# Kernel optimization log

Hardware: AMD Instinct MI355X
Metric: run time of the kernel (lower is better)

## Reference

```python
import jax, jax.numpy as jnp
import numpy as np
import math

COND_DIM = 64
HIDDEN = 128
NUM_SIN = 2
SQRT2 = 1.4142135623730951


def fused_leaky_relu(x, bias):
    # stylegan2 fused bias + leaky relu (slope 0.2) with sqrt(2) gain
    return jax.nn.leaky_relu(x + bias, negative_slope=0.2) * SQRT2


def equal_linear2(x, W, b, lr_mul=1.0, activation=False):
    scale = lr_mul / math.sqrt(W.shape[1])
    out = x @ (W * scale).T
    if activation:
        return fused_leaky_relu(out, b * lr_mul)
    return out + b * lr_mul


def coords_to_sinusoidals(x, num_sinusoidals=NUM_SIN, multiplier=2.0):
    # x: [P, 1] -> [P, 2*num_sinusoidals], freq_type='mult': freqs = multiplier**i
    freqs = multiplier ** jnp.arange(num_sinusoidals, dtype=x.dtype)  # [S]
    ang = x * freqs  # [P, S]
    return jnp.concatenate([jnp.sin(ang), jnp.cos(ang)], axis=-1)


def setup_inputs() -> dict:
    key = jax.random.key(0)
    ks = jax.random.split(key, 10)
    B, N = 64, 8192
    coord_in = 2 * NUM_SIN  # 4
    in1 = coord_in + COND_DIM  # 68
    in2 = HIDDEN + COND_DIM    # 192
    coords = jax.random.normal(ks[0], (B, N, 2), dtype=jnp.float32)
    c = jax.random.normal(ks[1], (B, N, COND_DIM), dtype=jnp.float32)
    # EqualLinear2 weights init uniform(-1,1)/lr_mul; last layer zero in torch,
    # use small random values here so gradients/outputs are non-trivial.
    Wx1 = jax.random.uniform(ks[2], (HIDDEN, in1), minval=-1.0, maxval=1.0)
    bx1 = jnp.zeros((HIDDEN,), jnp.float32)
    Wx2 = jax.random.uniform(ks[3], (2, in2), minval=-1.0, maxval=1.0) * 0.1
    bx2 = jnp.zeros((2,), jnp.float32)
    Wy1 = jax.random.uniform(ks[4], (HIDDEN, in1), minval=-1.0, maxval=1.0)
    by1 = jnp.zeros((HIDDEN,), jnp.float32)
    Wy2 = jax.random.uniform(ks[5], (2, in2), minval=-1.0, maxval=1.0) * 0.1
    by2 = jnp.zeros((2,), jnp.float32)
    return {"coords": coords, "c": c,
            "Wx1": Wx1, "bx1": bx1, "Wx2": Wx2, "bx2": bx2,
            "Wy1": Wy1, "by1": by1, "Wy2": Wy2, "by2": by2}


def reference(coords, c, Wx1, bx1, Wx2, bx2, Wy1, by1, Wy2, by2):
    initial_shape = coords.shape[:-1]
    coords2 = coords.reshape(-1, coords.shape[-1])  # [P, 2]
    cf = c.reshape(-1, c.shape[-1])                 # [P, cond]
    x = coords2[:, 0:1]
    y = coords2[:, 1:2]

    # x branch -> affine params for y
    h = coords_to_sinusoidals(x / 10.0)
    h = equal_linear2(jnp.concatenate([h, cf], -1), Wx1, bx1, activation=True)
    o = equal_linear2(jnp.concatenate([h, cf], -1), Wx2, bx2, activation=False)
    y_log_scale = jnp.clip(o[:, 0:1], -5.0, 5.0)
    y_bias = o[:, 1:2]
    y = y * jnp.exp(y_log_scale) + y_bias

    # y branch -> affine params for x
    h = coords_to_sinusoidals(y / 10.0)
    h = equal_linear2(jnp.concatenate([h, cf], -1), Wy1, by1, activation=True)
    o = equal_linear2(jnp.concatenate([h, cf], -1), Wy2, by2, activation=False)
    x_log_scale = jnp.clip(o[:, 0:1], -5.0, 5.0)
    x_bias = o[:, 1:2]
    x = x * jnp.exp(x_log_scale) + x_bias

    warped = jnp.concatenate([x, y], -1).reshape(*initial_shape, -1)
    log_jac = jnp.concatenate([x_log_scale + y_log_scale], -1)
    log_jac = (x_log_scale + y_log_scale).reshape(*initial_shape, -1)
    return warped, log_jac
```

## Files before the change

kernel.cpp:

```cpp
#include <hip/hip_runtime.h>

typedef unsigned short u16t;
typedef short short8 __attribute__((ext_vector_type(8)));
typedef float f32x4 __attribute__((ext_vector_type(4)));
typedef float f32x2 __attribute__((ext_vector_type(2)));

__device__ __forceinline__ u16t f2bf_rne(float f) {
  unsigned u = __builtin_bit_cast(unsigned, f);
  u += 0x7FFFu + ((u >> 16) & 1u);
  return (u16t)(u >> 16);
}
__device__ __forceinline__ unsigned pk2(float a, float b) {
  unsigned ua = __builtin_bit_cast(unsigned, a) + 0x8000u;
  unsigned ub = __builtin_bit_cast(unsigned, b) + 0x8000u;
  return (ua >> 16) | (ub & 0xFFFF0000u);
}
union S8U { short8 s; unsigned w[4]; };
__device__ __forceinline__ short8 pack8f(float4 a, float4 b) {
  S8U u;
  u.w[0] = pk2(a.x, a.y); u.w[1] = pk2(a.z, a.w);
  u.w[2] = pk2(b.x, b.y); u.w[3] = pk2(b.z, b.w);
  return u.s;
}

#define WS_WB  0
#define WS_BS  32768
#define WS_FQ  36864
#define LDS_BYTES 39936
#define WS_BC  39936
#define WS_BYTES 44032

__global__ void prep_kernel(const float* __restrict__ Wx1, const float* __restrict__ bx1,
                            const float* __restrict__ Wx2,
                            const float* __restrict__ Wy1, const float* __restrict__ by1,
                            const float* __restrict__ Wy2,
                            char* __restrict__ ws)
{
  const int b = blockIdx.x;
  const int lane = threadIdx.x;
  const int p = b >> 3, nt = b & 7;
  const int l15 = lane & 15, quad = lane >> 4;
  const float* W1 = p ? Wy1 : Wx1;
  const float* B1 = p ? by1 : bx1;
  const float* W2 = p ? Wy2 : Wx2;
  const int n = nt * 16 + l15;
  const float* rp = W1 + n * 68;
  short8 bb0, bb1;
  #pragma unroll
  for (int j = 0; j < 8; ++j) {
    bb0[j] = (short)f2bf_rne(rp[4 + quad * 8 + j]);
    bb1[j] = (short)f2bf_rne(rp[36 + quad * 8 + j]);
  }
  short8* wb = (short8*)(ws + WS_WB);
  wb[((p * 8 + nt) * 2 + 0) * 64 + lane] = bb0;
  wb[((p * 8 + nt) * 2 + 1) * 64 + lane] = bb1;

  if (quad == 0) {
    short8 t = (short8)0;
    #pragma unroll
    for (int j = 0; j < 4; ++j) t[j] = (short)f2bf_rne(rp[j]);
    ((short8*)(ws + WS_BS))[(p * 8 + nt) * 16 + l15] = t;
  }

  if (lane < 12) {
    const int q = lane / 3, t = lane - q * 3;
    const float SQ2 = 1.41421356237309515f;
    const float s1 = 0.121267812518166f;
    const float inv_s1 = 8.24621125123532110f;
    float4 v;
    #pragma unroll
    for (int j = 0; j < 4; ++j) {
      const int nn = nt * 16 + q * 4 + j;
      float val = (t == 0) ? B1[nn] * inv_s1
                : (t == 1) ? W2[nn] * SQ2 * s1
                           : W2[192 + nn] * SQ2 * s1;
      ((float*)&v)[j] = val;
    }
    ((float4*)(ws + WS_FQ))[((p * 8 + nt) * 4 + q) * 3 + t] = v;
  }

  if (b < 4) {
    const int p2 = b >> 1, h = b & 1;
    const float* W2b = p2 ? Wy2 : Wx2;
    short8 bc = (short8)0;
    if (l15 < 2) {
      #pragma unroll
      for (int j = 0; j < 8; ++j)
        bc[j] = (short)f2bf_rne(W2b[l15 * 192 + 128 + h * 32 + quad * 8 + j]);
    }
    ((short8*)(ws + WS_BC))[(p2 * 2 + h) * 64 + lane] = bc;
  }
}

__global__ __launch_bounds__(512, 2)
void icb_main(const float* __restrict__ g_coords, const float* __restrict__ g_c,
              const float* __restrict__ g_bx2, const float* __restrict__ g_by2,
              const char* __restrict__ ws, float* __restrict__ g_out)
{
  __shared__ float4 s_tab4[LDS_BYTES / 16];
  char* s_tab = (char*)s_tab4;

  const int tid  = threadIdx.x;
  const int lane = tid & 63, wave = tid >> 6;
  const int l15  = lane & 15, quad = lane >> 4;
  const int wbase = blockIdx.x * 256 + wave * 32;

  float4 ra[2][4]; float2 rco[2];
  #pragma unroll
  for (int mt = 0; mt < 2; ++mt) {
    const int r = wbase + mt * 16 + l15;
    const float4* cr = (const float4*)(g_c + (size_t)r * 64);
    ra[mt][0] = cr[quad * 2];     ra[mt][1] = cr[quad * 2 + 1];
    ra[mt][2] = cr[8 + quad * 2]; ra[mt][3] = cr[8 + quad * 2 + 1];
    rco[mt] = ((const float2*)g_coords)[r];
  }

  {
    const float4* src = (const float4*)ws;
    #pragma unroll
    for (int k = 0; k < 5; ++k) {
      const int t = tid + k * 512;
      if (t < LDS_BYTES / 16) s_tab4[t] = src[t];
    }
  }

  short8 aC0[2], aC1[2];
  float xold[2], yold[2];
  #pragma unroll
  for (int mt = 0; mt < 2; ++mt) {
    aC0[mt] = pack8f(ra[mt][0], ra[mt][1]);
    aC1[mt] = pack8f(ra[mt][2], ra[mt][3]);
    xold[mt] = rco[mt].x; yold[mt] = rco[mt].y;
  }

  __syncthreads();

  const short8* wb  = (const short8*)(s_tab + WS_WB);
  const short8* wbs = (const short8*)(s_tab + WS_BS);
  const f32x4*  wfq = (const f32x4*) (s_tab + WS_FQ);
  const short8* wbc = (const short8*)(ws + WS_BC);

  const float s2 = 0.0721687836487032f;

  float vin[2], xnew[2], ynew[2], xls[2], yls[2];
  vin[0] = xold[0]; vin[1] = xold[1];

  #pragma unroll 1
  for (int path = 0; path < 2; ++path) {
    const int pb = path * 8;
    const float* b2 = path ? g_by2 : g_bx2;
    const float b20 = b2[0], b21 = b2[1];

    short8 bc0 = wbc[(path * 2 + 0) * 64 + lane];
    short8 bc1 = wbc[(path * 2 + 1) * 64 + lane];

    short8 aS[2];
    #pragma unroll
    for (int mt = 0; mt < 2; ++mt) {
      short8 f = (short8)0;
      if (quad == 0) {
        float a = vin[mt] * 0.1f;
        float sa, ca;
        __sincosf(a, &sa, &ca);
        float s2a = 2.0f * sa * ca;
        float c2a = 1.0f - 2.0f * sa * sa;
        f[0] = (short)f2bf_rne(sa); f[1] = (short)f2bf_rne(s2a);
        f[2] = (short)f2bf_rne(ca); f[3] = (short)f2bf_rne(c2a);
      }
      aS[mt] = f;
    }

    f32x2 hp0[2], hp1[2];
    #pragma unroll
    for (int mt = 0; mt < 2; ++mt) { hp0[mt] = (f32x2)0.f; hp1[mt] = (f32x2)0.f; }

    #pragma unroll 2
    for (int nt = 0; nt < 8; ++nt) {
      short8 bb0 = wb[((pb + nt) * 2 + 0) * 64 + lane];
      short8 bb1 = wb[((pb + nt) * 2 + 1) * 64 + lane];
      short8 bsw = wbs[(pb + nt) * 16 + l15];
      const f32x4* fq = wfq + ((pb + nt) * 4 + quad) * 3;
      f32x4 cq = fq[0], w0q = fq[1], w1q = fq[2];
      f32x2 w0lo = {w0q[0], w0q[1]}, w0hi = {w0q[2], w0q[3]};
      f32x2 w1lo = {w1q[0], w1q[1]}, w1hi = {w1q[2], w1q[3]};
      #pragma unroll
      for (int mt = 0; mt < 2; ++mt) {
        f32x4 acc = cq;
        acc = __builtin_amdgcn_mfma_f32_16x16x32_bf16(bb0, aC0[mt], acc, 0, 0, 0);
        acc = __builtin_amdgcn_mfma_f32_16x16x32_bf16(bb1, aC1[mt], acc, 0, 0, 0);
        acc = __builtin_amdgcn_mfma_f32_16x16x32_bf16(bsw, aS[mt],  acc, 0, 0, 0);
        f32x2 dlo = {acc[0], acc[1]}, dhi = {acc[2], acc[3]};
        f32x2 mlo = __builtin_elementwise_max(dlo, dlo * 0.2f);
        f32x2 mhi = __builtin_elementwise_max(dhi, dhi * 0.2f);
        hp0[mt] = __builtin_elementwise_fma(mlo, w0lo, hp0[mt]);
        hp0[mt] = __builtin_elementwise_fma(mhi, w0hi, hp0[mt]);
        hp1[mt] = __builtin_elementwise_fma(mlo, w1lo, hp1[mt]);
        hp1[mt] = __builtin_elementwise_fma(mhi, w1hi, hp1[mt]);
      }
    }

    f32x4 acc8[2];
    #pragma unroll
    for (int mt = 0; mt < 2; ++mt) {
      f32x4 a = {0.f, 0.f, 0.f, 0.f};
      a = __builtin_amdgcn_mfma_f32_16x16x32_bf16(bc0, aC0[mt], a, 0, 0, 0);
      a = __builtin_amdgcn_mfma_f32_16x16x32_bf16(bc1, aC1[mt], a, 0, 0, 0);
      acc8[mt] = a;
    }

    #pragma unroll
    for (int mt = 0; mt < 2; ++mt) {
      float h0 = hp0[mt][0] + hp0[mt][1] + acc8[mt][0];
      float h1 = hp1[mt][0] + hp1[mt][1] + acc8[mt][1];
      h0 += __shfl_xor(h0, 16); h0 += __shfl_xor(h0, 32);
      h1 += __shfl_xor(h1, 16); h1 += __shfl_xor(h1, 32);

      float lsraw = fmaf(s2, h0, b20);
      float brow  = fmaf(s2, h1, b21);
      float ls = fminf(fmaxf(lsraw, -5.f), 5.f);
      float e  = __expf(ls);
      if (path == 0) {
        yls[mt]  = ls;
        ynew[mt] = fmaf(yold[mt], e, brow);
        vin[mt]  = ynew[mt];
      } else {
        xls[mt]  = ls;
        xnew[mt] = fmaf(xold[mt], e, brow);
      }
    }
  }

  if (lane < 16) {
    #pragma unroll
    for (int mt = 0; mt < 2; ++mt) {
      int R = wbase + mt * 16 + lane;
      float2 pw; pw.x = xnew[mt]; pw.y = ynew[mt];
      reinterpret_cast<float2*>(g_out)[R] = pw;
      g_out[1048576 + R] = xls[mt] + yls[mt];
    }
  }
}

extern "C" void kernel_launch(void* const* d_in, const int* in_sizes, int n_in,
                              void* d_out, int out_size, void* d_ws, size_t ws_size,
                              hipStream_t stream) {
  (void)in_sizes; (void)n_in; (void)out_size; (void)ws_size;
  prep_kernel<<<16, 64, 0, stream>>>(
      (const float*)d_in[2], (const float*)d_in[3], (const float*)d_in[4],
      (const float*)d_in[6], (const float*)d_in[7], (const float*)d_in[8],
      (char*)d_ws);
  icb_main<<<2048, 512, 0, stream>>>(
      (const float*)d_in[0], (const float*)d_in[1],
      (const float*)d_in[5], (const float*)d_in[9],
      (const char*)d_ws, (float*)d_out);
}
```

Measured before the change: 224.9 us.

## Stream layer-1 weights from global, shrink LDS table, raise occupancy

```diff
diff --git a/kernel.cpp b/kernel.cpp
--- a/kernel.cpp
+++ b/kernel.cpp
@@ -23,10 +23,10 @@
   return u.s;
 }
 
-#define WS_WB  0
-#define WS_BS  32768
-#define WS_FQ  36864
-#define LDS_BYTES 39936
+#define WS_BS  0
+#define WS_FQ  4096
+#define LDS_BYTES 7168
+#define WS_WB  7168
 #define WS_BC  39936
 #define WS_BYTES 44032
 
@@ -68,13 +68,14 @@
     const float s1 = 0.121267812518166f;
     const float inv_s1 = 8.24621125123532110f;
     float4 v;
-    #pragma unroll
-    for (int j = 0; j < 4; ++j) {
-      const int nn = nt * 16 + q * 4 + j;
-      float val = (t == 0) ? B1[nn] * inv_s1
-                : (t == 1) ? W2[nn] * SQ2 * s1
-                           : W2[192 + nn] * SQ2 * s1;
-      ((float*)&v)[j] = val;
+    if (t == 0) {
+      #pragma unroll
+      for (int j = 0; j < 4; ++j) v.x = 0, ((float*)&v)[j] = B1[nt * 16 + q * 4 + j] * inv_s1;
+    } else {
+      const int j0 = (t - 1) * 2;
+      const int n0 = nt * 16 + q * 4 + j0, n1 = n0 + 1;
+      v.x = W2[n0] * SQ2 * s1;  v.y = W2[192 + n0] * SQ2 * s1;
+      v.z = W2[n1] * SQ2 * s1;  v.w = W2[192 + n1] * SQ2 * s1;
     }
     ((float4*)(ws + WS_FQ))[((p * 8 + nt) * 4 + q) * 3 + t] = v;
   }
@@ -92,7 +93,7 @@
   }
 }
 
-__global__ __launch_bounds__(512, 2)
+__global__ __launch_bounds__(512, 4)
 void icb_main(const float* __restrict__ g_coords, const float* __restrict__ g_c,
               const float* __restrict__ g_bx2, const float* __restrict__ g_by2,
               const char* __restrict__ ws, float* __restrict__ g_out)
@@ -115,14 +116,7 @@
     rco[mt] = ((const float2*)g_coords)[r];
   }
 
-  {
-    const float4* src = (const float4*)ws;
-    #pragma unroll
-    for (int k = 0; k < 5; ++k) {
-      const int t = tid + k * 512;
-      if (t < LDS_BYTES / 16) s_tab4[t] = src[t];
-    }
-  }
+  if (tid < LDS_BYTES / 16) s_tab4[tid] = ((const float4*)ws)[tid];
 
   short8 aC0[2], aC1[2];
   float xold[2], yold[2];
@@ -135,9 +129,9 @@
 
   __syncthreads();
 
-  const short8* wb  = (const short8*)(s_tab + WS_WB);
   const short8* wbs = (const short8*)(s_tab + WS_BS);
   const f32x4*  wfq = (const f32x4*) (s_tab + WS_FQ);
+  const short8* wbg = (const short8*)(ws + WS_WB);
   const short8* wbc = (const short8*)(ws + WS_BC);
 
   const float s2 = 0.0721687836487032f;
@@ -170,32 +164,31 @@
       aS[mt] = f;
     }
 
-    f32x2 hp0[2], hp1[2];
-    #pragma unroll
-    for (int mt = 0; mt < 2; ++mt) { hp0[mt] = (f32x2)0.f; hp1[mt] = (f32x2)0.f; }
+    f32x2 hp[2];
+    hp[0] = (f32x2)0.f; hp[1] = (f32x2)0.f;
 
     #pragma unroll 2
     for (int nt = 0; nt < 8; ++nt) {
-      short8 bb0 = wb[((pb + nt) * 2 + 0) * 64 + lane];
-      short8 bb1 = wb[((pb + nt) * 2 + 1) * 64 + lane];
+      short8 bb0 = wbg[((pb + nt) * 2 + 0) * 64 + lane];
+      short8 bb1 = wbg[((pb + nt) * 2 + 1) * 64 + lane];
       short8 bsw = wbs[(pb + nt) * 16 + l15];
       const f32x4* fq = wfq + ((pb + nt) * 4 + quad) * 3;
-      f32x4 cq = fq[0], w0q = fq[1], w1q = fq[2];
-      f32x2 w0lo = {w0q[0], w0q[1]}, w0hi = {w0q[2], w0q[3]};
-      f32x2 w1lo = {w1q[0], w1q[1]}, w1hi = {w1q[2], w1q[3]};
+      f32x4 cq = fq[0], wA4 = fq[1], wB4 = fq[2];
+      f32x2 wA = {wA4[0], wA4[1]}, wB = {wA4[2], wA4[3]};
+      f32x2 wC = {wB4[0], wB4[1]}, wD = {wB4[2], wB4[3]};
       #pragma unroll
       for (int mt = 0; mt < 2; ++mt) {
         f32x4 acc = cq;
         acc = __builtin_amdgcn_mfma_f32_16x16x32_bf16(bb0, aC0[mt], acc, 0, 0, 0);
         acc = __builtin_amdgcn_mfma_f32_16x16x32_bf16(bb1, aC1[mt], acc, 0, 0, 0);
         acc = __builtin_amdgcn_mfma_f32_16x16x32_bf16(bsw, aS[mt],  acc, 0, 0, 0);
-        f32x2 dlo = {acc[0], acc[1]}, dhi = {acc[2], acc[3]};
-        f32x2 mlo = __builtin_elementwise_max(dlo, dlo * 0.2f);
-        f32x2 mhi = __builtin_elementwise_max(dhi, dhi * 0.2f);
-        hp0[mt] = __builtin_elementwise_fma(mlo, w0lo, hp0[mt]);
-        hp0[mt] = __builtin_elementwise_fma(mhi, w0hi, hp0[mt]);
-        hp1[mt] = __builtin_elementwise_fma(mlo, w1lo, hp1[mt]);
-        hp1[mt] = __builtin_elementwise_fma(mhi, w1hi, hp1[mt]);
+        f32x2 d01 = {acc[0], acc[1]}, d23 = {acc[2], acc[3]};
+        f32x2 m01 = __builtin_elementwise_max(d01, d01 * 0.2f);
+        f32x2 m23 = __builtin_elementwise_max(d23, d23 * 0.2f);
+        hp[mt] = __builtin_elementwise_fma((f32x2){m01[0], m01[0]}, wA, hp[mt]);
+        hp[mt] = __builtin_elementwise_fma((f32x2){m01[1], m01[1]}, wB, hp[mt]);
+        hp[mt] = __builtin_elementwise_fma((f32x2){m23[0], m23[0]}, wC, hp[mt]);
+        hp[mt] = __builtin_elementwise_fma((f32x2){m23[1], m23[1]}, wD, hp[mt]);
       }
     }
 
@@ -210,8 +203,8 @@
 
     #pragma unroll
     for (int mt = 0; mt < 2; ++mt) {
-      float h0 = hp0[mt][0] + hp0[mt][1] + acc8[mt][0];
-      float h1 = hp1[mt][0] + hp1[mt][1] + acc8[mt][1];
+      float h0 = hp[mt][0] + acc8[mt][0];
+      float h1 = hp[mt][1] + acc8[mt][1];
       h0 += __shfl_xor(h0, 16); h0 += __shfl_xor(h0, 32);
       h1 += __shfl_xor(h1, 16); h1 += __shfl_xor(h1, 32);
 
```

Measured after the change: 234.6 us. 1.04x slower.

## Make main kernel persistent over four tiles with register prefetch of next tile

Applied to the files above, without the earlier changes.

```diff
diff --git a/kernel.cpp b/kernel.cpp
--- a/kernel.cpp
+++ b/kernel.cpp
@@ -92,6 +92,32 @@
   }
 }
 
+struct LoadBuf { float4 a[8]; float2 co[2]; };
+struct Frags  { short8 c0[2], c1[2]; float xo[2], yo[2]; };
+
+__device__ __forceinline__ void issue_tile(LoadBuf& b, const float* __restrict__ g_c,
+                                           const float* __restrict__ g_coords,
+                                           int base, int l15, int quad) {
+  #pragma unroll
+  for (int mt = 0; mt < 2; ++mt) {
+    const int r = base + mt * 16 + l15;
+    const float4* cr = (const float4*)(g_c + (size_t)r * 64);
+    b.a[mt * 4 + 0] = cr[quad * 2];     b.a[mt * 4 + 1] = cr[quad * 2 + 1];
+    b.a[mt * 4 + 2] = cr[8 + quad * 2]; b.a[mt * 4 + 3] = cr[8 + quad * 2 + 1];
+    b.co[mt] = ((const float2*)g_coords)[r];
+  }
+}
+__device__ __forceinline__ void pack_tile(Frags& f, const LoadBuf& b) {
+  #pragma unroll
+  for (int mt = 0; mt < 2; ++mt) {
+    f.c0[mt] = pack8f(b.a[mt * 4 + 0], b.a[mt * 4 + 1]);
+    f.c1[mt] = pack8f(b.a[mt * 4 + 2], b.a[mt * 4 + 3]);
+    f.xo[mt] = b.co[mt].x; f.yo[mt] = b.co[mt].y;
+  }
+}
+
+#define NBLK  512
+#define TILES 4
 __global__ __launch_bounds__(512, 2)
 void icb_main(const float* __restrict__ g_coords, const float* __restrict__ g_c,
               const float* __restrict__ g_bx2, const float* __restrict__ g_by2,
@@ -103,18 +129,11 @@
   const int tid  = threadIdx.x;
   const int lane = tid & 63, wave = tid >> 6;
   const int l15  = lane & 15, quad = lane >> 4;
-  const int wbase = blockIdx.x * 256 + wave * 32;
-
-  float4 ra[2][4]; float2 rco[2];
-  #pragma unroll
-  for (int mt = 0; mt < 2; ++mt) {
-    const int r = wbase + mt * 16 + l15;
-    const float4* cr = (const float4*)(g_c + (size_t)r * 64);
-    ra[mt][0] = cr[quad * 2];     ra[mt][1] = cr[quad * 2 + 1];
-    ra[mt][2] = cr[8 + quad * 2]; ra[mt][3] = cr[8 + quad * 2 + 1];
-    rco[mt] = ((const float2*)g_coords)[r];
-  }
-
+  const int gwave = blockIdx.x * 8 + wave;
+  const int wstride = NBLK * 8;
+
+  LoadBuf buf;
+  issue_tile(buf, g_c, g_coords, gwave * 32, l15, quad);
   {
     const float4* src = (const float4*)ws;
     #pragma unroll
@@ -123,16 +142,8 @@
       if (t < LDS_BYTES / 16) s_tab4[t] = src[t];
     }
   }
-
-  short8 aC0[2], aC1[2];
-  float xold[2], yold[2];
-  #pragma unroll
-  for (int mt = 0; mt < 2; ++mt) {
-    aC0[mt] = pack8f(ra[mt][0], ra[mt][1]);
-    aC1[mt] = pack8f(ra[mt][2], ra[mt][3]);
-    xold[mt] = rco[mt].x; yold[mt] = rco[mt].y;
-  }
-
+  Frags fr;
+  pack_tile(fr, buf);
   __syncthreads();
 
   const short8* wb  = (const short8*)(s_tab + WS_WB);
@@ -141,103 +152,116 @@
   const short8* wbc = (const short8*)(ws + WS_BC);
 
   const float s2 = 0.0721687836487032f;
-
-  float vin[2], xnew[2], ynew[2], xls[2], yls[2];
-  vin[0] = xold[0]; vin[1] = xold[1];
-
-  #pragma unroll 1
-  for (int path = 0; path < 2; ++path) {
-    const int pb = path * 8;
-    const float* b2 = path ? g_by2 : g_bx2;
-    const float b20 = b2[0], b21 = b2[1];
-
-    short8 bc0 = wbc[(path * 2 + 0) * 64 + lane];
-    short8 bc1 = wbc[(path * 2 + 1) * 64 + lane];
-
-    short8 aS[2];
-    #pragma unroll
-    for (int mt = 0; mt < 2; ++mt) {
-      short8 f = (short8)0;
-      if (quad == 0) {
-        float a = vin[mt] * 0.1f;
-        float sa, ca;
-        __sincosf(a, &sa, &ca);
-        float s2a = 2.0f * sa * ca;
-        float c2a = 1.0f - 2.0f * sa * sa;
-        f[0] = (short)f2bf_rne(sa); f[1] = (short)f2bf_rne(s2a);
-        f[2] = (short)f2bf_rne(ca); f[3] = (short)f2bf_rne(c2a);
-      }
-      aS[mt] = f;
-    }
-
-    f32x2 hp0[2], hp1[2];
-    #pragma unroll
-    for (int mt = 0; mt < 2; ++mt) { hp0[mt] = (f32x2)0.f; hp1[mt] = (f32x2)0.f; }
-
-    #pragma unroll 2
-    for (int nt = 0; nt < 8; ++nt) {
-      short8 bb0 = wb[((pb + nt) * 2 + 0) * 64 + lane];
-      short8 bb1 = wb[((pb + nt) * 2 + 1) * 64 + lane];
-      short8 bsw = wbs[(pb + nt) * 16 + l15];
-      const f32x4* fq = wfq + ((pb + nt) * 4 + quad) * 3;
-      f32x4 cq = fq[0], w0q = fq[1], w1q = fq[2];
-      f32x2 w0lo = {w0q[0], w0q[1]}, w0hi = {w0q[2], w0q[3]};
-      f32x2 w1lo = {w1q[0], w1q[1]}, w1hi = {w1q[2], w1q[3]};
-      #pragma unroll
-      for (int mt = 0; mt < 2; ++mt) {
-        f32x4 acc = cq;
-        acc = __builtin_amdgcn_mfma_f32_16x16x32_bf16(bb0, aC0[mt], acc, 0, 0, 0);
-        acc = __builtin_amdgcn_mfma_f32_16x16x32_bf16(bb1, aC1[mt], acc, 0, 0, 0);
-        acc = __builtin_amdgcn_mfma_f32_16x16x32_bf16(bsw, aS[mt],  acc, 0, 0, 0);
-        f32x2 dlo = {acc[0], acc[1]}, dhi = {acc[2], acc[3]};
-        f32x2 mlo = __builtin_elementwise_max(dlo, dlo * 0.2f);
-        f32x2 mhi = __builtin_elementwise_max(dhi, dhi * 0.2f);
-        hp0[mt] = __builtin_elementwise_fma(mlo, w0lo, hp0[mt]);
-        hp0[mt] = __builtin_elementwise_fma(mhi, w0hi, hp0[mt]);
-        hp1[mt] = __builtin_elementwise_fma(mlo, w1lo, hp1[mt]);
-        hp1[mt] = __builtin_elementwise_fma(mhi, w1hi, hp1[mt]);
-      }
-    }
-
-    f32x4 acc8[2];
-    #pragma unroll
-    for (int mt = 0; mt < 2; ++mt) {
-      f32x4 a = {0.f, 0.f, 0.f, 0.f};
-      a = __builtin_amdgcn_mfma_f32_16x16x32_bf16(bc0, aC0[mt], a, 0, 0, 0);
-      a = __builtin_amdgcn_mfma_f32_16x16x32_bf16(bc1, aC1[mt], a, 0, 0, 0);
-      acc8[mt] = a;
-    }
-
-    #pragma unroll
-    for (int mt = 0; mt < 2; ++mt) {
-      float h0 = hp0[mt][0] + hp0[mt][1] + acc8[mt][0];
-      float h1 = hp1[mt][0] + hp1[mt][1] + acc8[mt][1];
-      h0 += __shfl_xor(h0, 16); h0 += __shfl_xor(h0, 32);
-      h1 += __shfl_xor(h1, 16); h1 += __shfl_xor(h1, 32);
-
-      float lsraw = fmaf(s2, h0, b20);
-      float brow  = fmaf(s2, h1, b21);
-      float ls = fminf(fmaxf(lsraw, -5.f), 5.f);
-      float e  = __expf(ls);
-      if (path == 0) {
-        yls[mt]  = ls;
-        ynew[mt] = fmaf(yold[mt], e, brow);
-        vin[mt]  = ynew[mt];
-      } else {
-        xls[mt]  = ls;
-        xnew[mt] = fmaf(xold[mt], e, brow);
-      }
-    }
-  }
-
-  if (lane < 16) {
-    #pragma unroll
-    for (int mt = 0; mt < 2; ++mt) {
-      int R = wbase + mt * 16 + lane;
-      float2 pw; pw.x = xnew[mt]; pw.y = ynew[mt];
-      reinterpret_cast<float2*>(g_out)[R] = pw;
-      g_out[1048576 + R] = xls[mt] + yls[mt];
-    }
+  const float gb20x = g_bx2[0], gb21x = g_bx2[1];
+  const float gb20y = g_by2[0], gb21y = g_by2[1];
+
+  #pragma unroll
+  for (int it = 0; it < TILES; ++it) {
+    const int wbase = (it * wstride + gwave) * 32;
+
+    if (it + 1 < TILES)
+      issue_tile(buf, g_c, g_coords, ((it + 1) * wstride + gwave) * 32, l15, quad);
+
+    float vin[2], xnew[2], ynew[2], xls[2], yls[2];
+    float xold[2] = {fr.xo[0], fr.xo[1]}, yold[2] = {fr.yo[0], fr.yo[1]};
+    short8 aC0[2] = {fr.c0[0], fr.c0[1]}, aC1[2] = {fr.c1[0], fr.c1[1]};
+    vin[0] = xold[0]; vin[1] = xold[1];
+
+    #pragma unroll 1
+    for (int path = 0; path < 2; ++path) {
+      const int pb = path * 8;
+      const float b20 = path ? gb20y : gb20x;
+      const float b21 = path ? gb21y : gb21x;
+
+      short8 bc0 = wbc[(path * 2 + 0) * 64 + lane];
+      short8 bc1 = wbc[(path * 2 + 1) * 64 + lane];
+
+      short8 aS[2];
+      #pragma unroll
+      for (int mt = 0; mt < 2; ++mt) {
+        short8 f = (short8)0;
+        if (quad == 0) {
+          float a = vin[mt] * 0.1f;
+          float sa, ca;
+          __sincosf(a, &sa, &ca);
+          float s2a = 2.0f * sa * ca;
+          float c2a = 1.0f - 2.0f * sa * sa;
+          f[0] = (short)f2bf_rne(sa); f[1] = (short)f2bf_rne(s2a);
+          f[2] = (short)f2bf_rne(ca); f[3] = (short)f2bf_rne(c2a);
+        }
+        aS[mt] = f;
+      }
+
+      f32x2 hp0[2], hp1[2];
+      #pragma unroll
+      for (int mt = 0; mt < 2; ++mt) { hp0[mt] = (f32x2)0.f; hp1[mt] = (f32x2)0.f; }
+
+      #pragma unroll 2
+      for (int nt = 0; nt < 8; ++nt) {
+        short8 bb0 = wb[((pb + nt) * 2 + 0) * 64 + lane];
+        short8 bb1 = wb[((pb + nt) * 2 + 1) * 64 + lane];
+        short8 bsw = wbs[(pb + nt) * 16 + l15];
+        const f32x4* fq = wfq + ((pb + nt) * 4 + quad) * 3;
+        f32x4 cq = fq[0], w0q = fq[1], w1q = fq[2];
+        f32x2 w0lo = {w0q[0], w0q[1]}, w0hi = {w0q[2], w0q[3]};
+        f32x2 w1lo = {w1q[0], w1q[1]}, w1hi = {w1q[2], w1q[3]};
+        #pragma unroll
+        for (int mt = 0; mt < 2; ++mt) {
+          f32x4 acc = cq;
+          acc = __builtin_amdgcn_mfma_f32_16x16x32_bf16(bb0, aC0[mt], acc, 0, 0, 0);
+          acc = __builtin_amdgcn_mfma_f32_16x16x32_bf16(bb1, aC1[mt], acc, 0, 0, 0);
+          acc = __builtin_amdgcn_mfma_f32_16x16x32_bf16(bsw, aS[mt],  acc, 0, 0, 0);
+          f32x2 dlo = {acc[0], acc[1]}, dhi = {acc[2], acc[3]};
+          f32x2 mlo = __builtin_elementwise_max(dlo, dlo * 0.2f);
+          f32x2 mhi = __builtin_elementwise_max(dhi, dhi * 0.2f);
+          hp0[mt] = __builtin_elementwise_fma(mlo, w0lo, hp0[mt]);
+          hp0[mt] = __builtin_elementwise_fma(mhi, w0hi, hp0[mt]);
+          hp1[mt] = __builtin_elementwise_fma(mlo, w1lo, hp1[mt]);
+          hp1[mt] = __builtin_elementwise_fma(mhi, w1hi, hp1[mt]);
+        }
+      }
+
+      f32x4 acc8[2];
+      #pragma unroll
+      for (int mt = 0; mt < 2; ++mt) {
+        f32x4 a = {0.f, 0.f, 0.f, 0.f};
+        a = __builtin_amdgcn_mfma_f32_16x16x32_bf16(bc0, aC0[mt], a, 0, 0, 0);
+        a = __builtin_amdgcn_mfma_f32_16x16x32_bf16(bc1, aC1[mt], a, 0, 0, 0);
+        acc8[mt] = a;
+      }
+
+      #pragma unroll
+      for (int mt = 0; mt < 2; ++mt) {
+        float h0 = hp0[mt][0] + hp0[mt][1] + acc8[mt][0];
+        float h1 = hp1[mt][0] + hp1[mt][1] + acc8[mt][1];
+        h0 += __shfl_xor(h0, 16); h0 += __shfl_xor(h0, 32);
+        h1 += __shfl_xor(h1, 16); h1 += __shfl_xor(h1, 32);
+
+        float lsraw = fmaf(s2, h0, b20);
+        float brow  = fmaf(s2, h1, b21);
+        float ls = fminf(fmaxf(lsraw, -5.f), 5.f);
+        float e  = __expf(ls);
+        if (path == 0) {
+          yls[mt]  = ls;
+          ynew[mt] = fmaf(yold[mt], e, brow);
+          vin[mt]  = ynew[mt];
+        } else {
+          xls[mt]  = ls;
+          xnew[mt] = fmaf(xold[mt], e, brow);
+        }
+      }
+    }
+
+    if (lane < 16) {
+      #pragma unroll
+      for (int mt = 0; mt < 2; ++mt) {
+        int R = wbase + mt * 16 + lane;
+        float2 pw; pw.x = xnew[mt]; pw.y = ynew[mt];
+        reinterpret_cast<float2*>(g_out)[R] = pw;
+        g_out[1048576 + R] = xls[mt] + yls[mt];
+      }
+    }
+    if (it + 1 < TILES) pack_tile(fr, buf);
   }
 }
 
@@ -249,7 +273,7 @@
       (const float*)d_in[2], (const float*)d_in[3], (const float*)d_in[4],
       (const float*)d_in[6], (const float*)d_in[7], (const float*)d_in[8],
       (char*)d_ws);
-  icb_main<<<2048, 512, 0, stream>>>(
+  icb_main<<<NBLK, 512, 0, stream>>>(
       (const float*)d_in[0], (const float*)d_in[1],
       (const float*)d_in[5], (const float*)d_in[9],
       (const char*)d_ws, (float*)d_out);
```

Measured after the change: 226.8 us. About the same (+0.8%).

## Fold layer-1 bias into sinusoid MFMA and hoist second-layer weight loads

Applied to the files above, without the earlier changes.

```diff
diff --git a/kernel.cpp b/kernel.cpp
--- a/kernel.cpp
+++ b/kernel.cpp
@@ -26,9 +26,9 @@
 #define WS_WB  0
 #define WS_BS  32768
 #define WS_FQ  36864
-#define LDS_BYTES 39936
-#define WS_BC  39936
-#define WS_BYTES 44032
+#define LDS_BYTES 38912
+#define WS_BC  38912
+#define WS_BYTES 43008
 
 __global__ void prep_kernel(const float* __restrict__ Wx1, const float* __restrict__ bx1,
                             const float* __restrict__ Wx2,
@@ -56,27 +56,25 @@
   wb[((p * 8 + nt) * 2 + 1) * 64 + lane] = bb1;
 
   if (quad == 0) {
+    const float inv_s1 = 8.24621125123532110f;
     short8 t = (short8)0;
     #pragma unroll
     for (int j = 0; j < 4; ++j) t[j] = (short)f2bf_rne(rp[j]);
+    t[4] = (short)f2bf_rne(B1[n] * inv_s1);
     ((short8*)(ws + WS_BS))[(p * 8 + nt) * 16 + l15] = t;
   }
 
-  if (lane < 12) {
-    const int q = lane / 3, t = lane - q * 3;
+  if (lane < 8) {
+    const int q = lane >> 1, t = lane & 1;
     const float SQ2 = 1.41421356237309515f;
     const float s1 = 0.121267812518166f;
-    const float inv_s1 = 8.24621125123532110f;
     float4 v;
     #pragma unroll
     for (int j = 0; j < 4; ++j) {
       const int nn = nt * 16 + q * 4 + j;
-      float val = (t == 0) ? B1[nn] * inv_s1
-                : (t == 1) ? W2[nn] * SQ2 * s1
-                           : W2[192 + nn] * SQ2 * s1;
-      ((float*)&v)[j] = val;
-    }
-    ((float4*)(ws + WS_FQ))[((p * 8 + nt) * 4 + q) * 3 + t] = v;
+      ((float*)&v)[j] = W2[(t ? 192 : 0) + nn] * SQ2 * s1;
+    }
+    ((float4*)(ws + WS_FQ))[((p * 8 + nt) * 4 + q) * 2 + t] = v;
   }
 
   if (b < 4) {
@@ -124,6 +122,12 @@
     }
   }
 
+  const short8* wbc = (const short8*)(ws + WS_BC);
+  short8 bcA0 = wbc[0 * 64 + lane], bcA1 = wbc[1 * 64 + lane];
+  short8 bcB0 = wbc[2 * 64 + lane], bcB1 = wbc[3 * 64 + lane];
+  const float gb20x = g_bx2[0], gb21x = g_bx2[1];
+  const float gb20y = g_by2[0], gb21y = g_by2[1];
+
   short8 aC0[2], aC1[2];
   float xold[2], yold[2];
   #pragma unroll
@@ -138,21 +142,19 @@
   const short8* wb  = (const short8*)(s_tab + WS_WB);
   const short8* wbs = (const short8*)(s_tab + WS_BS);
   const f32x4*  wfq = (const f32x4*) (s_tab + WS_FQ);
-  const short8* wbc = (const short8*)(ws + WS_BC);
 
   const float s2 = 0.0721687836487032f;
 
   float vin[2], xnew[2], ynew[2], xls[2], yls[2];
   vin[0] = xold[0]; vin[1] = xold[1];
 
-  #pragma unroll 1
+  #pragma unroll
   for (int path = 0; path < 2; ++path) {
     const int pb = path * 8;
-    const float* b2 = path ? g_by2 : g_bx2;
-    const float b20 = b2[0], b21 = b2[1];
-
-    short8 bc0 = wbc[(path * 2 + 0) * 64 + lane];
-    short8 bc1 = wbc[(path * 2 + 1) * 64 + lane];
+    const float b20 = path ? gb20y : gb20x;
+    const float b21 = path ? gb21y : gb21x;
+    const short8 bc0 = path ? bcB0 : bcA0;
+    const short8 bc1 = path ? bcB1 : bcA1;
 
     short8 aS[2];
     #pragma unroll
@@ -166,26 +168,33 @@
         float c2a = 1.0f - 2.0f * sa * sa;
         f[0] = (short)f2bf_rne(sa); f[1] = (short)f2bf_rne(s2a);
         f[2] = (short)f2bf_rne(ca); f[3] = (short)f2bf_rne(c2a);
+        f[4] = (short)0x3F80;
       }
       aS[mt] = f;
     }
 
     f32x2 hp0[2], hp1[2];
     #pragma unroll
-    for (int mt = 0; mt < 2; ++mt) { hp0[mt] = (f32x2)0.f; hp1[mt] = (f32x2)0.f; }
+    for (int mt = 0; mt < 2; ++mt) {
+      f32x4 a = {0.f, 0.f, 0.f, 0.f};
+      a = __builtin_amdgcn_mfma_f32_16x16x32_bf16(bc0, aC0[mt], a, 0, 0, 0);
+      a = __builtin_amdgcn_mfma_f32_16x16x32_bf16(bc1, aC1[mt], a, 0, 0, 0);
+      hp0[mt][0] = a[0]; hp0[mt][1] = 0.f;
+      hp1[mt][0] = a[1]; hp1[mt][1] = 0.f;
+    }
 
     #pragma unroll 2
     for (int nt = 0; nt < 8; ++nt) {
       short8 bb0 = wb[((pb + nt) * 2 + 0) * 64 + lane];
       short8 bb1 = wb[((pb + nt) * 2 + 1) * 64 + lane];
       short8 bsw = wbs[(pb + nt) * 16 + l15];
-      const f32x4* fq = wfq + ((pb + nt) * 4 + quad) * 3;
-      f32x4 cq = fq[0], w0q = fq[1], w1q = fq[2];
+      const f32x4* fq = wfq + ((pb + nt) * 4 + quad) * 2;
+      f32x4 w0q = fq[0], w1q = fq[1];
       f32x2 w0lo = {w0q[0], w0q[1]}, w0hi = {w0q[2], w0q[3]};
       f32x2 w1lo = {w1q[0], w1q[1]}, w1hi = {w1q[2], w1q[3]};
       #pragma unroll
       for (int mt = 0; mt < 2; ++mt) {
-        f32x4 acc = cq;
+        f32x4 acc = {0.f, 0.f, 0.f, 0.f};
         acc = __builtin_amdgcn_mfma_f32_16x16x32_bf16(bb0, aC0[mt], acc, 0, 0, 0);
         acc = __builtin_amdgcn_mfma_f32_16x16x32_bf16(bb1, aC1[mt], acc, 0, 0, 0);
         acc = __builtin_amdgcn_mfma_f32_16x16x32_bf16(bsw, aS[mt],  acc, 0, 0, 0);
@@ -199,19 +208,10 @@
       }
     }
 
-    f32x4 acc8[2];
-    #pragma unroll
-    for (int mt = 0; mt < 2; ++mt) {
-      f32x4 a = {0.f, 0.f, 0.f, 0.f};
-      a = __builtin_amdgcn_mfma_f32_16x16x32_bf16(bc0, aC0[mt], a, 0, 0, 0);
-      a = __builtin_amdgcn_mfma_f32_16x16x32_bf16(bc1, aC1[mt], a, 0, 0, 0);
-      acc8[mt] = a;
-    }
-
-    #pragma unroll
-    for (int mt = 0; mt < 2; ++mt) {
-      float h0 = hp0[mt][0] + hp0[mt][1] + acc8[mt][0];
-      float h1 = hp1[mt][0] + hp1[mt][1] + acc8[mt][1];
+    #pragma unroll
+    for (int mt = 0; mt < 2; ++mt) {
+      float h0 = hp0[mt][0] + hp0[mt][1];
+      float h1 = hp1[mt][0] + hp1[mt][1];
       h0 += __shfl_xor(h0, 16); h0 += __shfl_xor(h0, 32);
       h1 += __shfl_xor(h1, 16); h1 += __shfl_xor(h1, 32);
 
```

After: 229.7 us. +2.1%, slower.
